# Kernel tuning notes

Hardware: AMD Instinct MI355X
Metric: run time of the kernel (lower is better)

## Reference

```python
import jax
import jax.numpy as jnp
from jax import lax
import numpy as np

BATCH = 8192
FEATURE_DIM = 512
NUM_ATOMS = 4096
SPARSITY = 32


def setup_inputs() -> dict:
    key = jax.random.key(0)
    k1, k2 = jax.random.split(key)
    X = jax.random.normal(k1, (BATCH, FEATURE_DIM), dtype=jnp.float32)
    # xavier_uniform for [feature_dim, num_atoms]
    limit = float(np.sqrt(6.0 / (FEATURE_DIM + NUM_ATOMS)))
    dictionary = jax.random.uniform(
        k2, (FEATURE_DIM, NUM_ATOMS), dtype=jnp.float32, minval=-limit, maxval=limit
    )
    return {"X": X, "dictionary": dictionary, "sparsity": SPARSITY}


def _matching_pursuit_codes(x, D, sparsity):
    # x: [feature_dim], D: [feature_dim, num_atoms]
    num_atoms = D.shape[1]

    def step(carry, _):
        residual, codes = carry
        proj = residual @ D                      # [num_atoms]
        best = jnp.argmax(jnp.abs(proj))         # data-dependent atom pick
        coef = proj[best]
        codes = codes.at[best].add(coef)
        residual = residual - coef * lax.dynamic_index_in_dim(D, best, axis=1, keepdims=False)
        return (residual, codes), None

    init = (x, jnp.zeros((num_atoms,), dtype=x.dtype))
    (_, codes), _ = lax.scan(step, init, None, length=sparsity)
    return codes


def reference(X, dictionary, sparsity):
    # Greedy matching pursuit per sample, vectorized over the batch.
    codes = jax.vmap(lambda x: _matching_pursuit_codes(x, dictionary, sparsity))(X)
    # Original uses projections[best].item() -> codes are detached from autograd.
    codes = lax.stop_gradient(codes)
    recon = codes @ dictionary.T                 # [batch, feature_dim]
    return recon
```

## Files before the change

### kernel.cpp

```cpp
#include <hip/hip_runtime.h>


#define FD 512
#define NA 4096
#define NTHREAD 256
#define PR 16

#define TM 128
#define TN 128
#define TK 16
#define PADM 132

__global__ __launch_bounds__(1024) void k_transpose(const float* __restrict__ D,
                                                    float* __restrict__ DT) {
  __shared__ float tile[32][33];
  const int bx = blockIdx.x * 32;
  const int by = blockIdx.y * 32;
  const int tx = threadIdx.x, ty = threadIdx.y;
  tile[ty][tx] = D[(size_t)(by + ty) * NA + bx + tx];
  __syncthreads();
  DT[(size_t)(bx + ty) * FD + by + tx] = tile[tx][ty];
}

__global__ __launch_bounds__(256) void k_gemm_nn(const float* __restrict__ A,
                                                 const float* __restrict__ B,
                                                 float* __restrict__ C,
                                                 int M, int N, int K) {
  __shared__ float As[TK][PADM];
  __shared__ float Bs[TK][TN];
  const int t = threadIdx.x;
  const int tx = t & 15, ty = t >> 4;
  const int bm = blockIdx.y * TM, bn = blockIdx.x * TN;

  float acc[8][8];
#pragma unroll
  for (int i = 0; i < 8; i++)
#pragma unroll
    for (int j = 0; j < 8; j++) acc[i][j] = 0.f;

  for (int kt = 0; kt < K; kt += TK) {
#pragma unroll
    for (int i = 0; i < 2; i++) {
      const int f = t + i * 256;
      const int row = f >> 2;
      const int kc = (f & 3) * 4;
      const float4 v = *(const float4*)(A + (size_t)(bm + row) * K + kt + kc);
      As[kc + 0][row] = v.x;
      As[kc + 1][row] = v.y;
      As[kc + 2][row] = v.z;
      As[kc + 3][row] = v.w;
    }
#pragma unroll
    for (int i = 0; i < 2; i++) {
      const int f = t + i * 256;
      const int kr = f >> 5;
      const int nc = (f & 31) * 4;
      *(float4*)(&Bs[kr][nc]) = *(const float4*)(B + (size_t)(kt + kr) * N + bn + nc);
    }
    __syncthreads();
#pragma unroll
    for (int k = 0; k < TK; k++) {
      float a[8], b[8];
      *(float4*)(a) = *(const float4*)(&As[k][ty * 4]);
      *(float4*)(a + 4) = *(const float4*)(&As[k][64 + ty * 4]);
      *(float4*)(b) = *(const float4*)(&Bs[k][tx * 4]);
      *(float4*)(b + 4) = *(const float4*)(&Bs[k][64 + tx * 4]);
#pragma unroll
      for (int i = 0; i < 8; i++)
#pragma unroll
        for (int j = 0; j < 8; j++) acc[i][j] = fmaf(a[i], b[j], acc[i][j]);
    }
    __syncthreads();
  }
#pragma unroll
  for (int ih = 0; ih < 2; ih++)
#pragma unroll
    for (int i = 0; i < 4; i++) {
      float* Crow = C + (size_t)(bm + ih * 64 + ty * 4 + i) * N + bn;
      *(float4*)(Crow + tx * 4) = *(float4*)(&acc[ih * 4 + i][0]);
      *(float4*)(Crow + 64 + tx * 4) = *(float4*)(&acc[ih * 4 + i][4]);
    }
}

template <bool HAVE_PROJ>
__global__ __launch_bounds__(256) void k_mp(const float* __restrict__ X,
                                            const float* __restrict__ D,
                                            const float* __restrict__ proj_g,
                                            const float* __restrict__ G,
                                            const float* __restrict__ DT,
                                            float* __restrict__ out,
                                            const int* __restrict__ spars_p) {
  const int s = blockIdx.x;
  const int t = threadIdx.x;
  int sp = spars_p[0];
  if (sp > 64) sp = 64;
  if (sp < 0) sp = 0;

  __shared__ float red_abs[4];
  __shared__ int red_idx[4];
  __shared__ float coef_sh;
  __shared__ float xsh[FD];
  __shared__ int a_idx[64];
  __shared__ float a_coef[64];

  float p[PR];
  if (HAVE_PROJ) {
    const float* pr = proj_g + (size_t)s * NA;
#pragma unroll
    for (int r = 0; r < PR; r++) p[r] = pr[r * NTHREAD + t];
  } else {
    for (int i = t; i < FD; i += NTHREAD) xsh[i] = X[(size_t)s * FD + i];
    __syncthreads();
#pragma unroll
    for (int r = 0; r < PR; r++) p[r] = 0.f;
    for (int k = 0; k < FD; k++) {
      const float xv = xsh[k];
      const float* Drow = D + (size_t)k * NA;
#pragma unroll
      for (int r = 0; r < PR; r++) p[r] = fmaf(xv, Drow[r * NTHREAD + t], p[r]);
    }
  }

  for (int it = 0; it < sp; it++) {
    float ba = -1.f;
    int bi = 0x7fffffff;
#pragma unroll
    for (int r = 0; r < PR; r++) {
      const float av = fabsf(p[r]);
      const int idx = r * NTHREAD + t;
      if (av > ba || (av == ba && idx < bi)) {
        ba = av;
        bi = idx;
      }
    }
#pragma unroll
    for (int off = 32; off > 0; off >>= 1) {
      const float oa = __shfl_xor(ba, off);
      const int oi = __shfl_xor(bi, off);
      if (oa > ba || (oa == ba && oi < bi)) {
        ba = oa;
        bi = oi;
      }
    }
    if ((t & 63) == 0) {
      red_abs[t >> 6] = ba;
      red_idx[t >> 6] = bi;
    }
    __syncthreads();
    ba = red_abs[0];
    bi = red_idx[0];
#pragma unroll
    for (int w = 1; w < 4; w++) {
      const float oa = red_abs[w];
      const int oi = red_idx[w];
      if (oa > ba || (oa == ba && oi < bi)) {
        ba = oa;
        bi = oi;
      }
    }
    const int best = bi;
    if ((best & (NTHREAD - 1)) == t) {
      const float c = p[best >> 8];
      coef_sh = c;
      a_idx[it] = best;
      a_coef[it] = c;
    }
    __syncthreads();
    const float coef = coef_sh;
    const float* Grow = G + (size_t)best * NA;
#pragma unroll
    for (int r = 0; r < PR; r++) p[r] = fmaf(-coef, Grow[r * NTHREAD + t], p[r]);
  }

  __syncthreads();
  float2 acc = make_float2(0.f, 0.f);
  for (int it = 0; it < sp; it++) {
    const float c = a_coef[it];
    const float2 dv = *(const float2*)(DT + (size_t)a_idx[it] * FD + t * 2);
    acc.x = fmaf(c, dv.x, acc.x);
    acc.y = fmaf(c, dv.y, acc.y);
  }
  *(float2*)(out + (size_t)s * FD + t * 2) = acc;
}

extern "C" void kernel_launch(void* const* d_in, const int* in_sizes, int n_in,
                              void* d_out, int out_size, void* d_ws, size_t ws_size,
                              hipStream_t stream) {
  const float* X = (const float*)d_in[0];
  const float* D = (const float*)d_in[1];
  const int* spars = (const int*)d_in[2];
  float* out = (float*)d_out;
  const int B = in_sizes[0] / FD;

  char* ws = (char*)d_ws;
  float* DT = (float*)ws;
  float* G = (float*)(ws + (size_t)NA * FD * 4);
  float* proj = (float*)(ws + (size_t)NA * FD * 4 + (size_t)NA * NA * 4);
  const size_t need_full =
      (size_t)NA * FD * 4 + (size_t)NA * NA * 4 + (size_t)B * NA * 4;

  k_transpose<<<dim3(NA / 32, FD / 32), dim3(32, 32), 0, stream>>>(D, DT);
  k_gemm_nn<<<dim3(NA / TN, NA / TM), 256, 0, stream>>>(DT, D, G, NA, NA, FD);

  if (ws_size >= need_full) {
    k_gemm_nn<<<dim3(NA / TN, B / TM), 256, 0, stream>>>(X, D, proj, B, NA, FD);
    k_mp<true><<<B, NTHREAD, 0, stream>>>(X, D, proj, G, DT, out, spars);
  } else {
    k_mp<false><<<B, NTHREAD, 0, stream>>>(X, D, nullptr, G, DT, out, spars);
  }
}
```

Before: 1.232 ms.

## Run matching pursuit per sample in a single wavefront with fused argmax update

```diff
diff --git a/kernel.cpp b/kernel.cpp
--- a/kernel.cpp
+++ b/kernel.cpp
@@ -3,8 +3,6 @@
 
 #define FD 512
 #define NA 4096
-#define NTHREAD 256
-#define PR 16
 
 #define TM 128
 #define TN 128
@@ -83,104 +81,156 @@
 }
 
 template <bool HAVE_PROJ>
-__global__ __launch_bounds__(256) void k_mp(const float* __restrict__ X,
-                                            const float* __restrict__ D,
-                                            const float* __restrict__ proj_g,
-                                            const float* __restrict__ G,
-                                            const float* __restrict__ DT,
-                                            float* __restrict__ out,
-                                            const int* __restrict__ spars_p) {
+__global__ __launch_bounds__(64, 4) void k_mp64(const float* __restrict__ X,
+                                                const float* __restrict__ D,
+                                                const float* __restrict__ proj_g,
+                                                const float* __restrict__ G,
+                                                const float* __restrict__ DT,
+                                                float* __restrict__ out,
+                                                const int* __restrict__ spars_p) {
   const int s = blockIdx.x;
-  const int t = threadIdx.x;
+  const int l = threadIdx.x;
   int sp = spars_p[0];
-  if (sp > 64) sp = 64;
   if (sp < 0) sp = 0;
-
-  __shared__ float red_abs[4];
-  __shared__ int red_idx[4];
-  __shared__ float coef_sh;
+  if (sp > 128) sp = 128;
+
+  __shared__ int a_idx_sh[128];
+  __shared__ float a_coef_sh[128];
   __shared__ float xsh[FD];
-  __shared__ int a_idx[64];
-  __shared__ float a_coef[64];
-
-  float p[PR];
+
+  float p[64];
   if (HAVE_PROJ) {
-    const float* pr = proj_g + (size_t)s * NA;
-#pragma unroll
-    for (int r = 0; r < PR; r++) p[r] = pr[r * NTHREAD + t];
+    const float4* pr = (const float4*)(proj_g + (size_t)s * NA);
+#pragma unroll
+    for (int q = 0; q < 16; q++) {
+      const float4 v = pr[q * 64 + l];
+      p[q * 4 + 0] = v.x;
+      p[q * 4 + 1] = v.y;
+      p[q * 4 + 2] = v.z;
+      p[q * 4 + 3] = v.w;
+    }
   } else {
-    for (int i = t; i < FD; i += NTHREAD) xsh[i] = X[(size_t)s * FD + i];
+    for (int i = l; i < FD; i += 64) xsh[i] = X[(size_t)s * FD + i];
     __syncthreads();
 #pragma unroll
-    for (int r = 0; r < PR; r++) p[r] = 0.f;
+    for (int r = 0; r < 64; r++) p[r] = 0.f;
     for (int k = 0; k < FD; k++) {
       const float xv = xsh[k];
-      const float* Drow = D + (size_t)k * NA;
-#pragma unroll
-      for (int r = 0; r < PR; r++) p[r] = fmaf(xv, Drow[r * NTHREAD + t], p[r]);
+      const float4* Dr = (const float4*)(D + (size_t)k * NA);
+#pragma unroll
+      for (int q = 0; q < 16; q++) {
+        const float4 dv = Dr[q * 64 + l];
+        p[q * 4 + 0] = fmaf(xv, dv.x, p[q * 4 + 0]);
+        p[q * 4 + 1] = fmaf(xv, dv.y, p[q * 4 + 1]);
+        p[q * 4 + 2] = fmaf(xv, dv.z, p[q * 4 + 2]);
+        p[q * 4 + 3] = fmaf(xv, dv.w, p[q * 4 + 3]);
+      }
+    }
+  }
+
+  float av[4];
+  unsigned ap[4];
+#pragma unroll
+  for (int a = 0; a < 4; a++) {
+    av[a] = -1.f;
+    ap[a] = 0xffffffffu;
+  }
+#pragma unroll
+  for (int q = 0; q < 16; q++) {
+    const int a = q & 3;
+#pragma unroll
+    for (int j = 0; j < 4; j++) {
+      const float f = p[q * 4 + j];
+      const float af = fabsf(f);
+      const unsigned pay =
+          ((unsigned)(q * 256 + l * 4 + j) << 1) | (__float_as_uint(f) >> 31);
+      if (af > av[a]) {
+        av[a] = af;
+        ap[a] = pay;
+      }
     }
   }
 
   for (int it = 0; it < sp; it++) {
-    float ba = -1.f;
-    int bi = 0x7fffffff;
-#pragma unroll
-    for (int r = 0; r < PR; r++) {
-      const float av = fabsf(p[r]);
-      const int idx = r * NTHREAD + t;
-      if (av > ba || (av == ba && idx < bi)) {
-        ba = av;
-        bi = idx;
-      }
-    }
-#pragma unroll
-    for (int off = 32; off > 0; off >>= 1) {
-      const float oa = __shfl_xor(ba, off);
-      const int oi = __shfl_xor(bi, off);
-      if (oa > ba || (oa == ba && oi < bi)) {
-        ba = oa;
-        bi = oi;
-      }
-    }
-    if ((t & 63) == 0) {
-      red_abs[t >> 6] = ba;
-      red_idx[t >> 6] = bi;
-    }
-    __syncthreads();
-    ba = red_abs[0];
-    bi = red_idx[0];
-#pragma unroll
-    for (int w = 1; w < 4; w++) {
-      const float oa = red_abs[w];
-      const int oi = red_idx[w];
-      if (oa > ba || (oa == ba && oi < bi)) {
-        ba = oa;
-        bi = oi;
-      }
-    }
-    const int best = bi;
-    if ((best & (NTHREAD - 1)) == t) {
-      const float c = p[best >> 8];
-      coef_sh = c;
-      a_idx[it] = best;
-      a_coef[it] = c;
-    }
-    __syncthreads();
-    const float coef = coef_sh;
-    const float* Grow = G + (size_t)best * NA;
-#pragma unroll
-    for (int r = 0; r < PR; r++) p[r] = fmaf(-coef, Grow[r * NTHREAD + t], p[r]);
+    float fa = av[0];
+    unsigned pa = ap[0];
+#pragma unroll
+    for (int a = 1; a < 4; a++) {
+      if (av[a] > fa || (av[a] == fa && ap[a] < pa)) {
+        fa = av[a];
+        pa = ap[a];
+      }
+    }
+    unsigned long long key =
+        ((unsigned long long)__float_as_uint(fa) << 32) | (unsigned)(~pa);
+#pragma unroll
+    for (int off = 1; off < 64; off <<= 1) {
+      const unsigned long long ok = __shfl_xor(key, off);
+      if (ok > key) key = ok;
+    }
+    const unsigned pay = ~(unsigned)key;
+    const int best = pay >> 1;
+    const float ba = __uint_as_float((unsigned)(key >> 32));
+    const float coef = (pay & 1) ? -ba : ba;
+
+    if (l == 0) {
+      a_idx_sh[it] = best;
+      a_coef_sh[it] = coef;
+    }
+
+#pragma unroll
+    for (int a = 0; a < 4; a++) {
+      av[a] = -1.f;
+      ap[a] = 0xffffffffu;
+    }
+    const float4* Gr = (const float4*)(G + (size_t)best * NA);
+#pragma unroll
+    for (int h = 0; h < 2; h++) {
+      float4 g[8];
+#pragma unroll
+      for (int q = 0; q < 8; q++) g[q] = Gr[(h * 8 + q) * 64 + l];
+#pragma unroll
+      for (int q = 0; q < 8; q++) {
+        const int qq = h * 8 + q;
+        const int a = qq & 3;
+        float f0 = fmaf(-coef, g[q].x, p[qq * 4 + 0]);
+        float f1 = fmaf(-coef, g[q].y, p[qq * 4 + 1]);
+        float f2 = fmaf(-coef, g[q].z, p[qq * 4 + 2]);
+        float f3 = fmaf(-coef, g[q].w, p[qq * 4 + 3]);
+        p[qq * 4 + 0] = f0;
+        p[qq * 4 + 1] = f1;
+        p[qq * 4 + 2] = f2;
+        p[qq * 4 + 3] = f3;
+        const unsigned base = (unsigned)(qq * 256 + l * 4) << 1;
+        const float a0 = fabsf(f0), a1 = fabsf(f1), a2 = fabsf(f2), a3 = fabsf(f3);
+        if (a0 > av[a]) { av[a] = a0; ap[a] = base | 0 | (__float_as_uint(f0) >> 31); }
+        if (a1 > av[a]) { av[a] = a1; ap[a] = base | 2 | (__float_as_uint(f1) >> 31); }
+        if (a2 > av[a]) { av[a] = a2; ap[a] = base | 4 | (__float_as_uint(f2) >> 31); }
+        if (a3 > av[a]) { av[a] = a3; ap[a] = base | 6 | (__float_as_uint(f3) >> 31); }
+      }
+    }
   }
 
   __syncthreads();
-  float2 acc = make_float2(0.f, 0.f);
+  float4 acc0 = make_float4(0.f, 0.f, 0.f, 0.f);
+  float4 acc1 = make_float4(0.f, 0.f, 0.f, 0.f);
   for (int it = 0; it < sp; it++) {
-    const float c = a_coef[it];
-    const float2 dv = *(const float2*)(DT + (size_t)a_idx[it] * FD + t * 2);
-    acc.x = fmaf(c, dv.x, acc.x);
-    acc.y = fmaf(c, dv.y, acc.y);
-  }
-  *(float2*)(out + (size_t)s * FD + t * 2) = acc;
+    const float c = a_coef_sh[it];
+    const float4* dr = (const float4*)(DT + (size_t)a_idx_sh[it] * FD);
+    const float4 d0 = dr[l];
+    const float4 d1 = dr[64 + l];
+    acc0.x = fmaf(c, d0.x, acc0.x);
+    acc0.y = fmaf(c, d0.y, acc0.y);
+    acc0.z = fmaf(c, d0.z, acc0.z);
+    acc0.w = fmaf(c, d0.w, acc0.w);
+    acc1.x = fmaf(c, d1.x, acc1.x);
+    acc1.y = fmaf(c, d1.y, acc1.y);
+    acc1.z = fmaf(c, d1.z, acc1.z);
+    acc1.w = fmaf(c, d1.w, acc1.w);
+  }
+  float4* orow = (float4*)(out + (size_t)s * FD);
+  orow[l] = acc0;
+  orow[64 + l] = acc1;
 }
 
 extern "C" void kernel_launch(void* const* d_in, const int* in_sizes, int n_in,
@@ -204,8 +254,8 @@
 
   if (ws_size >= need_full) {
     k_gemm_nn<<<dim3(NA / TN, B / TM), 256, 0, stream>>>(X, D, proj, B, NA, FD);
-    k_mp<true><<<B, NTHREAD, 0, stream>>>(X, D, proj, G, DT, out, spars);
+    k_mp64<true><<<B, 64, 0, stream>>>(X, D, proj, G, DT, out, spars);
   } else {
-    k_mp<false><<<B, NTHREAD, 0, stream>>>(X, D, nullptr, G, DT, out, spars);
-  }
-}
+    k_mp64<false><<<B, 64, 0, stream>>>(X, D, nullptr, G, DT, out, spars);
+  }
+}
```

Measured after the change: 1.181 ms. 1.04x faster.
